# Performance work log

Measured on AMD Instinct MI355X. Metric: run time of the kernel, lower is better.

The kernel has to match this reference:

```python
import jax, jax.numpy as jnp
import numpy as np
from jax import lax

H = W = 1024

def _conv_sig(x, w, b):
    # 3x3 conv, padding=1 (SAME), NCHW / OIHW, followed by sigmoid
    y = lax.conv_general_dilated(x, w, (1, 1), 'SAME',
                                 dimension_numbers=('NCHW', 'OIHW', 'NCHW'))
    return jax.nn.sigmoid(y + b[None, :, None, None])


def setup_inputs() -> dict:
    key = jax.random.key(0)
    ks = jax.random.split(key, 20)
    d = {
        'x':  jax.random.normal(ks[0], (1, 3, H, W), jnp.float32),
        'x2': jax.random.normal(ks[1], (1, 3, H, W), jnp.float32),
        'w1a': jax.random.normal(ks[2], (1, 3, 3, 3), jnp.float32) * 0.1,
        'b1a': jax.random.normal(ks[3], (1,), jnp.float32) * 0.1,
        'w2a': jax.random.normal(ks[4], (1, 4, 3, 3), jnp.float32) * 0.1,
        'b2a': jax.random.normal(ks[5], (1,), jnp.float32) * 0.1,
        'w3a': jax.random.normal(ks[6], (1, 5, 3, 3), jnp.float32) * 0.1,
        'b3a': jax.random.normal(ks[7], (1,), jnp.float32) * 0.1,
        'w1b': jax.random.normal(ks[8], (1, 3, 3, 3), jnp.float32) * 0.1,
        'b1b': jax.random.normal(ks[9], (1,), jnp.float32) * 0.1,
        'w2b': jax.random.normal(ks[10], (1, 4, 3, 3), jnp.float32) * 0.1,
        'b2b': jax.random.normal(ks[11], (1,), jnp.float32) * 0.1,
        'w3b': jax.random.normal(ks[12], (1, 5, 3, 3), jnp.float32) * 0.1,
        'b3b': jax.random.normal(ks[13], (1,), jnp.float32) * 0.1,
        'lw1': jax.random.normal(ks[14], (128, 6), jnp.float32) * 0.1,
        'lb1': jax.random.normal(ks[15], (128,), jnp.float32) * 0.1,
        'lw2': jax.random.normal(ks[16], (2, 128), jnp.float32) * 0.1,
        'lb2': jax.random.normal(ks[17], (2,), jnp.float32) * 0.1,
    }
    return d


def _encode(x, params):
    # three stacked conv(3x3)+sigmoid blocks with densenet-style concat: C 3->4->5->6
    (w1, b1), (w2, b2), (w3, b3) = params
    x = jnp.concatenate([x, _conv_sig(x, w1, b1)], axis=1)
    x = jnp.concatenate([x, _conv_sig(x, w2, b2)], axis=1)
    x = jnp.concatenate([x, _conv_sig(x, w3, b3)], axis=1)
    return x  # [1, 6, H, W]


def reference(x, x2, w1a, b1a, w2a, b2a, w3a, b3a,
              w1b, b1b, w2b, b2b, w3b, b3b, lw1, lb1, lw2, lb2):
    # name branch: passthrough (3-channel input, e.g. name='opt')
    xa = _encode(x,  [(w1a, b1a), (w2a, b2a), (w3a, b3a)])
    xb = _encode(x2, [(w1b, b1b), (w2b, b2b), (w3b, b3b)])
    x3 = xa - xb                                   # [1, 6, H, W]
    feat = jnp.transpose(x3, (0, 2, 3, 1)).reshape(H * W, 6)
    feat = feat @ lw1.T + lb1                      # [HW, 128]
    outfeature = feat @ lw2.T + lb2                # [HW, 2]
    den_x1 = jnp.transpose(xa, (0, 2, 3, 1)).reshape(H, W, 6)
    den_x2 = jnp.transpose(xb, (0, 2, 3, 1)).reshape(H, W, 6)
    return outfeature, den_x1, den_x2
```

## Files before the change

### kernel.cpp

```cpp
#include <hip/hip_runtime.h>
#include <math.h>

#define IMG  1024
#define TS   32
#define HALO 3
#define XT   38
#define S1T  36
#define S2T  34

__device__ __forceinline__ float sigf(float y) {
    return 1.0f / (1.0f + __expf(-y));
}

__device__ __forceinline__ void acc9(float acc[4], const float v[6][3], const float* w9) {
#pragma unroll
    for (int dy = 0; dy < 3; ++dy)
#pragma unroll
        for (int dx = 0; dx < 3; ++dx) {
            float ww = w9[dy * 3 + dx];
#pragma unroll
            for (int rr = 0; rr < 4; ++rr)
                acc[rr] += ww * v[rr + dy][dx];
        }
}

__global__ __launch_bounds__(256, 4)
void unet_fused(const float* __restrict__ x, const float* __restrict__ x2,
                const float* __restrict__ w1a, const float* __restrict__ b1a,
                const float* __restrict__ w2a, const float* __restrict__ b2a,
                const float* __restrict__ w3a, const float* __restrict__ b3a,
                const float* __restrict__ w1b, const float* __restrict__ b1b,
                const float* __restrict__ w2b, const float* __restrict__ b2b,
                const float* __restrict__ w3b, const float* __restrict__ b3b,
                const float* __restrict__ lw1, const float* __restrict__ lb1,
                const float* __restrict__ lw2, const float* __restrict__ lb2,
                float* __restrict__ out)
{
    __shared__ float xt[3][XT * XT];
    __shared__ float s1[S1T * S1T];
    __shared__ float s2[S2T * S2T];
    __shared__ float wc[14];

    const int tid = threadIdx.x;
    const int bx = blockIdx.x, by = blockIdx.y;
    const int row0 = by * TS - HALO, col0 = bx * TS - HALO;

    const int c_out = tid & 31;
    const int r0_out = (tid >> 5) * 4;

    if (tid < 12) {
        int o = tid / 6, ch = tid % 6;
        float acc = 0.0f;
        for (int k = 0; k < 128; ++k) acc += lw2[o * 128 + k] * lw1[k * 6 + ch];
        wc[tid] = acc;
    } else if (tid < 14) {
        int o = tid - 12;
        float acc = lb2[o];
        for (int k = 0; k < 128; ++k) acc += lw2[o * 128 + k] * lb1[k];
        wc[tid] = acc;
    }

    const float* XS[2] = {x, x2};
    const float* W1[2] = {w1a, w1b};
    const float* W2[2] = {w2a, w2b};
    const float* W3[2] = {w3a, w3b};
    const float* B1[2] = {b1a, b1b};
    const float* B2[2] = {b2a, b2b};
    const float* B3[2] = {b3a, b3b};

    const long out1 = (long)2 * IMG * IMG;
    const long out2 = out1 + (long)6 * IMG * IMG;

    float areg[4][6];

#pragma unroll
    for (int br = 0; br < 2; ++br) {
        const float* xin = XS[br];
        for (int idx = tid; idx < 3 * XT * XT; idx += 256) {
            int pl = idx / (XT * XT);
            int i  = idx - pl * (XT * XT);
            int r = i / XT, cc = i - r * XT;
            int gr = row0 + r, gc = col0 + cc;
            bool ok = ((unsigned)gr < (unsigned)IMG) && ((unsigned)gc < (unsigned)IMG);
            float v = 0.0f;
            if (ok) v = xin[(long)pl * (IMG * IMG) + (long)gr * IMG + gc];
            xt[pl][i] = v;
        }
        __syncthreads();

        {
            float w[27];
#pragma unroll
            for (int i = 0; i < 27; ++i) w[i] = W1[br][i];
            const float bias = B1[br][0];
            for (int item = tid; item < S1T * 9; item += 256) {
                int c = item % S1T, rg = item / S1T;
                int r0 = rg * 4;
                float acc[4] = {bias, bias, bias, bias};
#pragma unroll
                for (int ic = 0; ic < 3; ++ic) {
                    const float* xp = &xt[ic][r0 * XT + c];
                    float v[6][3];
#pragma unroll
                    for (int rr = 0; rr < 6; ++rr)
#pragma unroll
                        for (int cc = 0; cc < 3; ++cc)
                            v[rr][cc] = xp[rr * XT + cc];
                    acc9(acc, v, &w[ic * 9]);
                }
                int gc1 = col0 + 1 + c;
                bool cok = (unsigned)gc1 < (unsigned)IMG;
                float* so = &s1[r0 * S1T + c];
#pragma unroll
                for (int rr = 0; rr < 4; ++rr) {
                    int gr1 = row0 + 1 + r0 + rr;
                    bool ok = cok && ((unsigned)gr1 < (unsigned)IMG);
                    so[rr * S1T] = ok ? sigf(acc[rr]) : 0.0f;
                }
            }
        }
        __syncthreads();

        {
            float w[36];
#pragma unroll
            for (int i = 0; i < 36; ++i) w[i] = W2[br][i];
            const float bias = B2[br][0];
            for (int item = tid; item < S2T * 9; item += 256) {
                int c = item % S2T, rg = item / S2T;
                int r0 = rg * 4;
                float acc[4] = {bias, bias, bias, bias};
#pragma unroll
                for (int ic = 0; ic < 3; ++ic) {
                    float v[6][3];
#pragma unroll
                    for (int rr = 0; rr < 6; ++rr) {
                        int rrow = r0 + 1 + rr; if (rrow > XT - 1) rrow = XT - 1;
#pragma unroll
                        for (int cc = 0; cc < 3; ++cc)
                            v[rr][cc] = xt[ic][rrow * XT + (c + 1 + cc)];
                    }
                    acc9(acc, v, &w[ic * 9]);
                }
                {
                    float v[6][3];
#pragma unroll
                    for (int rr = 0; rr < 6; ++rr) {
                        int rrow = r0 + rr; if (rrow > S1T - 1) rrow = S1T - 1;
#pragma unroll
                        for (int cc = 0; cc < 3; ++cc)
                            v[rr][cc] = s1[rrow * S1T + (c + cc)];
                    }
                    acc9(acc, v, &w[27]);
                }
                int gc2 = col0 + 2 + c;
                bool cok = (unsigned)gc2 < (unsigned)IMG;
                float* so = &s2[r0 * S2T + c];
#pragma unroll
                for (int rr = 0; rr < 4; ++rr) {
                    int srow = r0 + rr;
                    if (srow < S2T) {
                        int gr2 = row0 + 2 + srow;
                        bool ok = cok && ((unsigned)gr2 < (unsigned)IMG);
                        so[rr * S2T] = ok ? sigf(acc[rr]) : 0.0f;
                    }
                }
            }
        }
        __syncthreads();

        {
            float w[45];
#pragma unroll
            for (int i = 0; i < 45; ++i) w[i] = W3[br][i];
            const float bias = B3[br][0];
            const int c = c_out, r0 = r0_out;
            float acc[4] = {bias, bias, bias, bias};
#pragma unroll
            for (int ic = 0; ic < 3; ++ic) {
                float v[6][3];
#pragma unroll
                for (int rr = 0; rr < 6; ++rr)
#pragma unroll
                    for (int cc = 0; cc < 3; ++cc)
                        v[rr][cc] = xt[ic][(r0 + 2 + rr) * XT + (c + 2 + cc)];
                acc9(acc, v, &w[ic * 9]);
            }
            {
                float v[6][3];
#pragma unroll
                for (int rr = 0; rr < 6; ++rr)
#pragma unroll
                    for (int cc = 0; cc < 3; ++cc)
                        v[rr][cc] = s1[(r0 + 1 + rr) * S1T + (c + 1 + cc)];
                acc9(acc, v, &w[27]);
            }
            {
                float v[6][3];
#pragma unroll
                for (int rr = 0; rr < 6; ++rr)
#pragma unroll
                    for (int cc = 0; cc < 3; ++cc)
                        v[rr][cc] = s2[(r0 + rr) * S2T + (c + cc)];
                acc9(acc, v, &w[36]);
            }

            float cur[4][6];
#pragma unroll
            for (int rr = 0; rr < 4; ++rr) {
#pragma unroll
                for (int ch = 0; ch < 3; ++ch)
                    cur[rr][ch] = xt[ch][(r0 + 3 + rr) * XT + (c + 3)];
                cur[rr][3] = s1[(r0 + 2 + rr) * S1T + (c + 2)];
                cur[rr][4] = s2[(r0 + 1 + rr) * S2T + (c + 1)];
                cur[rr][5] = sigf(acc[rr]);
            }

            const long denOff = (br == 0) ? out1 : out2;
#pragma unroll
            for (int rr = 0; rr < 4; ++rr) {
                long gr = (long)by * TS + r0 + rr;
                long pix = gr * IMG + ((long)bx * TS + c);
                float* pd = out + denOff + pix * 6;
#pragma unroll
                for (int ch = 0; ch < 6; ++ch) pd[ch] = cur[rr][ch];
            }

            if (br == 0) {
#pragma unroll
                for (int rr = 0; rr < 4; ++rr)
#pragma unroll
                    for (int ch = 0; ch < 6; ++ch) areg[rr][ch] = cur[rr][ch];
            } else {
                float wcr[14];
#pragma unroll
                for (int i = 0; i < 14; ++i) wcr[i] = wc[i];
#pragma unroll
                for (int rr = 0; rr < 4; ++rr) {
                    float o0 = wcr[12], o1 = wcr[13];
#pragma unroll
                    for (int ch = 0; ch < 6; ++ch) {
                        float d = areg[rr][ch] - cur[rr][ch];
                        o0 += wcr[ch]     * d;
                        o1 += wcr[6 + ch] * d;
                    }
                    long gr = (long)by * TS + r0 + rr;
                    long pix = gr * IMG + ((long)bx * TS + c);
                    out[pix * 2]     = o0;
                    out[pix * 2 + 1] = o1;
                }
            }
        }
        __syncthreads();
    }
}

extern "C" void kernel_launch(void* const* d_in, const int* in_sizes, int n_in,
                              void* d_out, int out_size, void* d_ws, size_t ws_size,
                              hipStream_t stream) {
    const float* x   = (const float*)d_in[0];
    const float* x2  = (const float*)d_in[1];
    const float* w1a = (const float*)d_in[2];
    const float* b1a = (const float*)d_in[3];
    const float* w2a = (const float*)d_in[4];
    const float* b2a = (const float*)d_in[5];
    const float* w3a = (const float*)d_in[6];
    const float* b3a = (const float*)d_in[7];
    const float* w1b = (const float*)d_in[8];
    const float* b1b = (const float*)d_in[9];
    const float* w2b = (const float*)d_in[10];
    const float* b2b = (const float*)d_in[11];
    const float* w3b = (const float*)d_in[12];
    const float* b3b = (const float*)d_in[13];
    const float* lw1 = (const float*)d_in[14];
    const float* lb1 = (const float*)d_in[15];
    const float* lw2 = (const float*)d_in[16];
    const float* lb2 = (const float*)d_in[17];
    float* out = (float*)d_out;

    dim3 grid(IMG / TS, IMG / TS);
    unet_fused<<<grid, 256, 0, stream>>>(x, x2,
                                         w1a, b1a, w2a, b2a, w3a, b3a,
                                         w1b, b1b, w2b, b2b, w3b, b3b,
                                         lw1, lb1, lw2, lb2, out);
}
```

Baseline: 155.7 us.

## Rewrite fused conv kernel with 32x16 tiles, vectorized LDS and 2x4 register blocking

Replaces the 32x32 tile kernel with a 32x16 tile, 40-wide aligned shared buffers, float4 global and LDS loads for interior tiles, and per-thread 2x4 output blocking that reuses loaded rows across vertically adjacent outputs. It also remaps block IDs to spread neighbouring tiles, folds the branch-A projection into two partial sums instead of keeping six channels, vectorizes the output stores, and raises launch bounds to 6 blocks. The aim is to cut LDS traffic and redundant halo work and to raise occupancy. In exchange, fewer threads per block do compute (64 to 90 of 256), and smaller tiles have proportionally more halo.

New measurement: 253.1 us. 62.5% more time.

```diff
diff --git a/kernel.cpp b/kernel.cpp
--- a/kernel.cpp
+++ b/kernel.cpp
@@ -1,30 +1,301 @@
 #include <hip/hip_runtime.h>
-#include <math.h>
-
-#define IMG  1024
-#define TS   32
-#define HALO 3
-#define XT   38
-#define S1T  36
-#define S2T  34
-
-__device__ __forceinline__ float sigf(float y) {
-    return 1.0f / (1.0f + __expf(-y));
+
+#define IMG   1024
+#define TSW   32
+#define TSH   16
+#define XTW   40
+#define XTH   22
+#define SW    40
+#define S1H   20
+#define S2H   18
+
+#define OUT1  (2*IMG*IMG)
+#define OUT2  (OUT1 + 6*IMG*IMG)
+
+__device__ __forceinline__ float sigf(float y) { return 1.0f / (1.0f + __expf(-y)); }
+
+__device__ __forceinline__ void ld8(const float* p, float* w) {
+    float4 A = *(const float4*)p;
+    float4 B = *(const float4*)(p + 4);
+    w[0]=A.x; w[1]=A.y; w[2]=A.z; w[3]=A.w;
+    w[4]=B.x; w[5]=B.y; w[6]=B.z; w[7]=B.w;
 }
 
-__device__ __forceinline__ void acc9(float acc[4], const float v[6][3], const float* w9) {
-#pragma unroll
-    for (int dy = 0; dy < 3; ++dy)
-#pragma unroll
-        for (int dx = 0; dx < 3; ++dx) {
-            float ww = w9[dy * 3 + dx];
-#pragma unroll
-            for (int rr = 0; rr < 4; ++rr)
-                acc[rr] += ww * v[rr + dy][dx];
-        }
+template<int BR>
+__device__ __forceinline__ void do_branch(
+    const float* __restrict__ xin,
+    const float* __restrict__ w1, float b1,
+    const float* __restrict__ w2, float b2,
+    const float* __restrict__ w3, float b3,
+    float* xt, float* s1, float* s2, const float* wc,
+    int tid, int R0, int C0, bool edge,
+    float pa[2][4][2], float* __restrict__ out)
+{
+    if (!edge) {
+        for (int it = tid; it < 660; it += 256) {
+            int ch  = it / 220;  int rem = it - ch * 220;
+            int row = rem / 10;  int seg = rem - row * 10;
+            float4 v = *(const float4*)(xin + ch * (IMG*IMG) + (R0 - 3 + row) * IMG + (C0 - 4) + seg * 4);
+            *(float4*)(xt + ch * (XTH*XTW) + row * XTW + seg * 4) = v;
+        }
+    } else {
+        for (int it = tid; it < 3 * XTH * XTW; it += 256) {
+            int ch  = it / (XTH*XTW); int rem = it - ch * (XTH*XTW);
+            int row = rem / XTW;      int col = rem - row * XTW;
+            int gr = R0 - 3 + row, gc = C0 - 4 + col;
+            float v = 0.0f;
+            if ((unsigned)gr < (unsigned)IMG && (unsigned)gc < (unsigned)IMG)
+                v = xin[ch * (IMG*IMG) + gr * IMG + gc];
+            xt[it] = v;
+        }
+    }
+    __syncthreads();
+
+    if (tid < 90) {
+        int r = tid / 9, cg = tid - r * 9, c4 = cg * 4;
+        float acc[2][4];
+#pragma unroll
+        for (int q = 0; q < 2; ++q)
+#pragma unroll
+            for (int j = 0; j < 4; ++j) acc[q][j] = b1;
+#pragma unroll
+        for (int ch = 0; ch < 3; ++ch) {
+            float w9[9];
+#pragma unroll
+            for (int i = 0; i < 9; ++i) w9[i] = w1[ch * 9 + i];
+            const float* base = xt + ch * (XTH*XTW) + (2 * r) * XTW + c4;
+#pragma unroll
+            for (int dr = 0; dr < 4; ++dr) {
+                float w8[8]; ld8(base + dr * XTW, w8);
+#pragma unroll
+                for (int q = 0; q < 2; ++q) {
+                    const int dy = dr - q;
+                    if (dy >= 0 && dy < 3) {
+#pragma unroll
+                        for (int j = 0; j < 4; ++j)
+#pragma unroll
+                            for (int dx = 0; dx < 3; ++dx)
+                                acc[q][j] += w9[dy * 3 + dx] * w8[1 + j + dx];
+                    }
+                }
+            }
+        }
+        int gr0 = R0 - 2 + 2 * r, gc0 = C0 - 2 + c4;
+#pragma unroll
+        for (int q = 0; q < 2; ++q) {
+            bool rok = (unsigned)(gr0 + q) < (unsigned)IMG;
+            float o[4];
+#pragma unroll
+            for (int j = 0; j < 4; ++j) {
+                bool ok = rok && ((unsigned)(gc0 + j) < (unsigned)IMG);
+                o[j] = ok ? sigf(acc[q][j]) : 0.0f;
+            }
+            *(float4*)(s1 + (2 * r + q) * SW + c4) = make_float4(o[0], o[1], o[2], o[3]);
+        }
+    }
+    __syncthreads();
+
+    if (tid < 81) {
+        int r = tid / 9, cg = tid - r * 9, c4 = cg * 4;
+        float acc[2][4];
+#pragma unroll
+        for (int q = 0; q < 2; ++q)
+#pragma unroll
+            for (int j = 0; j < 4; ++j) acc[q][j] = b2;
+#pragma unroll
+        for (int ch = 0; ch < 3; ++ch) {
+            float w9[9];
+#pragma unroll
+            for (int i = 0; i < 9; ++i) w9[i] = w2[ch * 9 + i];
+            const float* base = xt + ch * (XTH*XTW) + (2 * r + 1) * XTW + c4;
+#pragma unroll
+            for (int dr = 0; dr < 4; ++dr) {
+                float w8[8]; ld8(base + dr * XTW, w8);
+#pragma unroll
+                for (int q = 0; q < 2; ++q) {
+                    const int dy = dr - q;
+                    if (dy >= 0 && dy < 3) {
+#pragma unroll
+                        for (int j = 0; j < 4; ++j)
+#pragma unroll
+                            for (int dx = 0; dx < 3; ++dx)
+                                acc[q][j] += w9[dy * 3 + dx] * w8[2 + j + dx];
+                    }
+                }
+            }
+        }
+        {
+            float w9[9];
+#pragma unroll
+            for (int i = 0; i < 9; ++i) w9[i] = w2[27 + i];
+            const float* base = s1 + (2 * r) * SW + c4;
+#pragma unroll
+            for (int dr = 0; dr < 4; ++dr) {
+                float w8[8]; ld8(base + dr * SW, w8);
+#pragma unroll
+                for (int q = 0; q < 2; ++q) {
+                    const int dy = dr - q;
+                    if (dy >= 0 && dy < 3) {
+#pragma unroll
+                        for (int j = 0; j < 4; ++j)
+#pragma unroll
+                            for (int dx = 0; dx < 3; ++dx)
+                                acc[q][j] += w9[dy * 3 + dx] * w8[j + dx];
+                    }
+                }
+            }
+        }
+        int gr0 = R0 - 1 + 2 * r, gc0 = C0 - 1 + c4;
+#pragma unroll
+        for (int q = 0; q < 2; ++q) {
+            bool rok = (unsigned)(gr0 + q) < (unsigned)IMG;
+            float o[4];
+#pragma unroll
+            for (int j = 0; j < 4; ++j) {
+                bool ok = rok && ((unsigned)(gc0 + j) < (unsigned)IMG);
+                o[j] = ok ? sigf(acc[q][j]) : 0.0f;
+            }
+            *(float4*)(s2 + (2 * r + q) * SW + c4) = make_float4(o[0], o[1], o[2], o[3]);
+        }
+    }
+    __syncthreads();
+
+    if (tid < 64) {
+        int r = tid >> 3, cg = tid & 7, c4 = cg * 4;
+        float acc[2][4];
+#pragma unroll
+        for (int q = 0; q < 2; ++q)
+#pragma unroll
+            for (int j = 0; j < 4; ++j) acc[q][j] = b3;
+#pragma unroll
+        for (int ch = 0; ch < 3; ++ch) {
+            float w9[9];
+#pragma unroll
+            for (int i = 0; i < 9; ++i) w9[i] = w3[ch * 9 + i];
+            const float* base = xt + ch * (XTH*XTW) + (2 * r + 2) * XTW + c4;
+#pragma unroll
+            for (int dr = 0; dr < 4; ++dr) {
+                const float* p = base + dr * XTW;
+                float2 A  = *(const float2*)(p + 2);
+                float4 B  = *(const float4*)(p + 4);
+                float2 Cx = *(const float2*)(p + 8);
+                float w8[8] = {A.x, A.y, B.x, B.y, B.z, B.w, Cx.x, Cx.y};
+#pragma unroll
+                for (int q = 0; q < 2; ++q) {
+                    const int dy = dr - q;
+                    if (dy >= 0 && dy < 3) {
+#pragma unroll
+                        for (int j = 0; j < 4; ++j)
+#pragma unroll
+                            for (int dx = 0; dx < 3; ++dx)
+                                acc[q][j] += w9[dy * 3 + dx] * w8[j + 1 + dx];
+                    }
+                }
+            }
+        }
+        {
+            float w9[9];
+#pragma unroll
+            for (int i = 0; i < 9; ++i) w9[i] = w3[27 + i];
+            const float* base = s1 + (2 * r + 1) * SW + c4;
+#pragma unroll
+            for (int dr = 0; dr < 4; ++dr) {
+                float w8[8]; ld8(base + dr * SW, w8);
+#pragma unroll
+                for (int q = 0; q < 2; ++q) {
+                    const int dy = dr - q;
+                    if (dy >= 0 && dy < 3) {
+#pragma unroll
+                        for (int j = 0; j < 4; ++j)
+#pragma unroll
+                            for (int dx = 0; dx < 3; ++dx)
+                                acc[q][j] += w9[dy * 3 + dx] * w8[1 + j + dx];
+                    }
+                }
+            }
+        }
+        {
+            float w9[9];
+#pragma unroll
+            for (int i = 0; i < 9; ++i) w9[i] = w3[36 + i];
+            const float* base = s2 + (2 * r) * SW + c4;
+#pragma unroll
+            for (int dr = 0; dr < 4; ++dr) {
+                float w8[8]; ld8(base + dr * SW, w8);
+#pragma unroll
+                for (int q = 0; q < 2; ++q) {
+                    const int dy = dr - q;
+                    if (dy >= 0 && dy < 3) {
+#pragma unroll
+                        for (int j = 0; j < 4; ++j)
+#pragma unroll
+                            for (int dx = 0; dx < 3; ++dx)
+                                acc[q][j] += w9[dy * 3 + dx] * w8[j + dx];
+                    }
+                }
+            }
+        }
+
+#pragma unroll
+        for (int q = 0; q < 2; ++q) {
+            float cur[4][6];
+#pragma unroll
+            for (int ch = 0; ch < 3; ++ch) {
+                float4 g = *(const float4*)(xt + ch * (XTH*XTW) + (2 * r + 3 + q) * XTW + c4 + 4);
+                cur[0][ch] = g.x; cur[1][ch] = g.y; cur[2][ch] = g.z; cur[3][ch] = g.w;
+            }
+            {
+                float2 a = *(const float2*)(s1 + (2 * r + 2 + q) * SW + c4 + 2);
+                float2 b = *(const float2*)(s1 + (2 * r + 2 + q) * SW + c4 + 4);
+                cur[0][3] = a.x; cur[1][3] = a.y; cur[2][3] = b.x; cur[3][3] = b.y;
+            }
+            {
+                float4 a = *(const float4*)(s2 + (2 * r + 1 + q) * SW + c4);
+                float  e = s2[(2 * r + 1 + q) * SW + c4 + 4];
+                cur[0][4] = a.y; cur[1][4] = a.z; cur[2][4] = a.w; cur[3][4] = e;
+            }
+#pragma unroll
+            for (int j = 0; j < 4; ++j) cur[j][5] = sigf(acc[q][j]);
+
+            const int pix0 = (R0 + 2 * r + q) * IMG + C0 + c4;
+            const int denOff = (BR == 0) ? OUT1 : OUT2;
+#pragma unroll
+            for (int j = 0; j < 4; ++j) {
+                float* pd = out + denOff + (pix0 + j) * 6;
+                *(float2*)(pd)     = make_float2(cur[j][0], cur[j][1]);
+                *(float2*)(pd + 2) = make_float2(cur[j][2], cur[j][3]);
+                *(float2*)(pd + 4) = make_float2(cur[j][4], cur[j][5]);
+            }
+            if (BR == 0) {
+#pragma unroll
+                for (int j = 0; j < 4; ++j) {
+                    float p0 = 0.0f, p1 = 0.0f;
+#pragma unroll
+                    for (int ch = 0; ch < 6; ++ch) {
+                        p0 += wc[ch]     * cur[j][ch];
+                        p1 += wc[6 + ch] * cur[j][ch];
+                    }
+                    pa[q][j][0] = p0; pa[q][j][1] = p1;
+                }
+            } else {
+#pragma unroll
+                for (int j = 0; j < 4; ++j) {
+                    float o0 = pa[q][j][0] + wc[12];
+                    float o1 = pa[q][j][1] + wc[13];
+#pragma unroll
+                    for (int ch = 0; ch < 6; ++ch) {
+                        o0 -= wc[ch]     * cur[j][ch];
+                        o1 -= wc[6 + ch] * cur[j][ch];
+                    }
+                    *(float2*)(out + (pix0 + j) * 2) = make_float2(o0, o1);
+                }
+            }
+        }
+    }
+    __syncthreads();
 }
 
-__global__ __launch_bounds__(256, 4)
+__global__ __launch_bounds__(256, 6)
 void unet_fused(const float* __restrict__ x, const float* __restrict__ x2,
                 const float* __restrict__ w1a, const float* __restrict__ b1a,
                 const float* __restrict__ w2a, const float* __restrict__ b2a,
@@ -36,20 +307,21 @@
                 const float* __restrict__ lw2, const float* __restrict__ lb2,
                 float* __restrict__ out)
 {
-    __shared__ float xt[3][XT * XT];
-    __shared__ float s1[S1T * S1T];
-    __shared__ float s2[S2T * S2T];
+    __shared__ float xt[3 * XTH * XTW];
+    __shared__ float s1[S1H * SW];
+    __shared__ float s2[S2H * SW];
     __shared__ float wc[14];
 
     const int tid = threadIdx.x;
-    const int bx = blockIdx.x, by = blockIdx.y;
-    const int row0 = by * TS - HALO, col0 = bx * TS - HALO;
-
-    const int c_out = tid & 31;
-    const int r0_out = (tid >> 5) * 4;
+
+    int lin = blockIdx.y * gridDim.x + blockIdx.x;
+    int nid = (lin & 7) * 256 + (lin >> 3);
+    int bx = nid & 31, by = nid >> 5;
+    const int R0 = by * TSH, C0 = bx * TSW;
+    const bool edge = (bx == 0) | (bx == 31) | (by == 0) | (by == 63);
 
     if (tid < 12) {
-        int o = tid / 6, ch = tid % 6;
+        int o = tid / 6, ch = tid - o * 6;
         float acc = 0.0f;
         for (int k = 0; k < 128; ++k) acc += lw2[o * 128 + k] * lw1[k * 6 + ch];
         wc[tid] = acc;
@@ -60,199 +332,12 @@
         wc[tid] = acc;
     }
 
-    const float* XS[2] = {x, x2};
-    const float* W1[2] = {w1a, w1b};
-    const float* W2[2] = {w2a, w2b};
-    const float* W3[2] = {w3a, w3b};
-    const float* B1[2] = {b1a, b1b};
-    const float* B2[2] = {b2a, b2b};
-    const float* B3[2] = {b3a, b3b};
-
-    const long out1 = (long)2 * IMG * IMG;
-    const long out2 = out1 + (long)6 * IMG * IMG;
-
-    float areg[4][6];
-
-#pragma unroll
-    for (int br = 0; br < 2; ++br) {
-        const float* xin = XS[br];
-        for (int idx = tid; idx < 3 * XT * XT; idx += 256) {
-            int pl = idx / (XT * XT);
-            int i  = idx - pl * (XT * XT);
-            int r = i / XT, cc = i - r * XT;
-            int gr = row0 + r, gc = col0 + cc;
-            bool ok = ((unsigned)gr < (unsigned)IMG) && ((unsigned)gc < (unsigned)IMG);
-            float v = 0.0f;
-            if (ok) v = xin[(long)pl * (IMG * IMG) + (long)gr * IMG + gc];
-            xt[pl][i] = v;
-        }
-        __syncthreads();
-
-        {
-            float w[27];
-#pragma unroll
-            for (int i = 0; i < 27; ++i) w[i] = W1[br][i];
-            const float bias = B1[br][0];
-            for (int item = tid; item < S1T * 9; item += 256) {
-                int c = item % S1T, rg = item / S1T;
-                int r0 = rg * 4;
-                float acc[4] = {bias, bias, bias, bias};
-#pragma unroll
-                for (int ic = 0; ic < 3; ++ic) {
-                    const float* xp = &xt[ic][r0 * XT + c];
-                    float v[6][3];
-#pragma unroll
-                    for (int rr = 0; rr < 6; ++rr)
-#pragma unroll
-                        for (int cc = 0; cc < 3; ++cc)
-                            v[rr][cc] = xp[rr * XT + cc];
-                    acc9(acc, v, &w[ic * 9]);
-                }
-                int gc1 = col0 + 1 + c;
-                bool cok = (unsigned)gc1 < (unsigned)IMG;
-                float* so = &s1[r0 * S1T + c];
-#pragma unroll
-                for (int rr = 0; rr < 4; ++rr) {
-                    int gr1 = row0 + 1 + r0 + rr;
-                    bool ok = cok && ((unsigned)gr1 < (unsigned)IMG);
-                    so[rr * S1T] = ok ? sigf(acc[rr]) : 0.0f;
-                }
-            }
-        }
-        __syncthreads();
-
-        {
-            float w[36];
-#pragma unroll
-            for (int i = 0; i < 36; ++i) w[i] = W2[br][i];
-            const float bias = B2[br][0];
-            for (int item = tid; item < S2T * 9; item += 256) {
-                int c = item % S2T, rg = item / S2T;
-                int r0 = rg * 4;
-                float acc[4] = {bias, bias, bias, bias};
-#pragma unroll
-                for (int ic = 0; ic < 3; ++ic) {
-                    float v[6][3];
-#pragma unroll
-                    for (int rr = 0; rr < 6; ++rr) {
-                        int rrow = r0 + 1 + rr; if (rrow > XT - 1) rrow = XT - 1;
-#pragma unroll
-                        for (int cc = 0; cc < 3; ++cc)
-                            v[rr][cc] = xt[ic][rrow * XT + (c + 1 + cc)];
-                    }
-                    acc9(acc, v, &w[ic * 9]);
-                }
-                {
-                    float v[6][3];
-#pragma unroll
-                    for (int rr = 0; rr < 6; ++rr) {
-                        int rrow = r0 + rr; if (rrow > S1T - 1) rrow = S1T - 1;
-#pragma unroll
-                        for (int cc = 0; cc < 3; ++cc)
-                            v[rr][cc] = s1[rrow * S1T + (c + cc)];
-                    }
-                    acc9(acc, v, &w[27]);
-                }
-                int gc2 = col0 + 2 + c;
-                bool cok = (unsigned)gc2 < (unsigned)IMG;
-                float* so = &s2[r0 * S2T + c];
-#pragma unroll
-                for (int rr = 0; rr < 4; ++rr) {
-                    int srow = r0 + rr;
-                    if (srow < S2T) {
-                        int gr2 = row0 + 2 + srow;
-                        bool ok = cok && ((unsigned)gr2 < (unsigned)IMG);
-                        so[rr * S2T] = ok ? sigf(acc[rr]) : 0.0f;
-                    }
-                }
-            }
-        }
-        __syncthreads();
-
-        {
-            float w[45];
-#pragma unroll
-            for (int i = 0; i < 45; ++i) w[i] = W3[br][i];
-            const float bias = B3[br][0];
-            const int c = c_out, r0 = r0_out;
-            float acc[4] = {bias, bias, bias, bias};
-#pragma unroll
-            for (int ic = 0; ic < 3; ++ic) {
-                float v[6][3];
-#pragma unroll
-                for (int rr = 0; rr < 6; ++rr)
-#pragma unroll
-                    for (int cc = 0; cc < 3; ++cc)
-                        v[rr][cc] = xt[ic][(r0 + 2 + rr) * XT + (c + 2 + cc)];
-                acc9(acc, v, &w[ic * 9]);
-            }
-            {
-                float v[6][3];
-#pragma unroll
-                for (int rr = 0; rr < 6; ++rr)
-#pragma unroll
-                    for (int cc = 0; cc < 3; ++cc)
-                        v[rr][cc] = s1[(r0 + 1 + rr) * S1T + (c + 1 + cc)];
-                acc9(acc, v, &w[27]);
-            }
-            {
-                float v[6][3];
-#pragma unroll
-                for (int rr = 0; rr < 6; ++rr)
-#pragma unroll
-                    for (int cc = 0; cc < 3; ++cc)
-                        v[rr][cc] = s2[(r0 + rr) * S2T + (c + cc)];
-                acc9(acc, v, &w[36]);
-            }
-
-            float cur[4][6];
-#pragma unroll
-            for (int rr = 0; rr < 4; ++rr) {
-#pragma unroll
-                for (int ch = 0; ch < 3; ++ch)
-                    cur[rr][ch] = xt[ch][(r0 + 3 + rr) * XT + (c + 3)];
-                cur[rr][3] = s1[(r0 + 2 + rr) * S1T + (c + 2)];
-                cur[rr][4] = s2[(r0 + 1 + rr) * S2T + (c + 1)];
-                cur[rr][5] = sigf(acc[rr]);
-            }
-
-            const long denOff = (br == 0) ? out1 : out2;
-#pragma unroll
-            for (int rr = 0; rr < 4; ++rr) {
-                long gr = (long)by * TS + r0 + rr;
-                long pix = gr * IMG + ((long)bx * TS + c);
-                float* pd = out + denOff + pix * 6;
-#pragma unroll
-                for (int ch = 0; ch < 6; ++ch) pd[ch] = cur[rr][ch];
-            }
-
-            if (br == 0) {
-#pragma unroll
-                for (int rr = 0; rr < 4; ++rr)
-#pragma unroll
-                    for (int ch = 0; ch < 6; ++ch) areg[rr][ch] = cur[rr][ch];
-            } else {
-                float wcr[14];
-#pragma unroll
-                for (int i = 0; i < 14; ++i) wcr[i] = wc[i];
-#pragma unroll
-                for (int rr = 0; rr < 4; ++rr) {
-                    float o0 = wcr[12], o1 = wcr[13];
-#pragma unroll
-                    for (int ch = 0; ch < 6; ++ch) {
-                        float d = areg[rr][ch] - cur[rr][ch];
-                        o0 += wcr[ch]     * d;
-                        o1 += wcr[6 + ch] * d;
-                    }
-                    long gr = (long)by * TS + r0 + rr;
-                    long pix = gr * IMG + ((long)bx * TS + c);
-                    out[pix * 2]     = o0;
-                    out[pix * 2 + 1] = o1;
-                }
-            }
-        }
-        __syncthreads();
-    }
+    float pa[2][4][2];
+
+    do_branch<0>(x,  w1a, b1a[0], w2a, b2a[0], w3a, b3a[0],
+                 xt, s1, s2, wc, tid, R0, C0, edge, pa, out);
+    do_branch<1>(x2, w1b, b1b[0], w2b, b2b[0], w3b, b3b[0],
+                 xt, s1, s2, wc, tid, R0, C0, edge, pa, out);
 }
 
 extern "C" void kernel_launch(void* const* d_in, const int* in_sizes, int n_in,
@@ -278,7 +363,7 @@
     const float* lb2 = (const float*)d_in[17];
     float* out = (float*)d_out;
 
-    dim3 grid(IMG / TS, IMG / TS);
+    dim3 grid(IMG / TSW, IMG / TSH);
     unet_fused<<<grid, 256, 0, stream>>>(x, x2,
                                          w1a, b1a, w2a, b2a, w3a, b3a,
                                          w1b, b1b, w2b, b2b, w3b, b3b,
```
